# Kernel optimization log

Hardware: AMD Instinct MI355X
Metric: run time of the kernel (lower is better)

Reference implementation:

```python
import jax, jax.numpy as jnp
import numpy as np

B, S, D, H = 4, 1024, 1024, 16
DH = D // H  # head dim = 64


def setup_inputs() -> dict:
    key = jax.random.key(0)
    k0, k1, k2 = jax.random.split(key, 3)
    x = jax.random.normal(k0, (B, S, D), dtype=jnp.float32)
    c_attn_w = jax.random.normal(k1, (D, 3 * D), dtype=jnp.float32) * 0.02
    c_attn_b = jnp.zeros((3 * D,), dtype=jnp.float32)
    c_proj_w = jax.random.normal(k2, (D, D), dtype=jnp.float32) * 0.02
    c_proj_b = jnp.zeros((D,), dtype=jnp.float32)
    return {"x": x, "c_attn_w": c_attn_w, "c_attn_b": c_attn_b,
            "c_proj_w": c_proj_w, "c_proj_b": c_proj_b}


def reference(x, c_attn_w, c_attn_b, c_proj_w, c_proj_b):
    b, s, d = x.shape
    # Conv1D (GPT-2 style): out = x @ W + b, fused QKV
    qkv = jnp.einsum('bsd,de->bse', x, c_attn_w) + c_attn_b
    q, k, v = jnp.split(qkv, 3, axis=-1)
    # split heads -> [b, h, s, dh]
    q = q.reshape(b, s, H, DH).transpose(0, 2, 1, 3)
    k = k.reshape(b, s, H, DH).transpose(0, 2, 1, 3)
    v = v.reshape(b, s, H, DH).transpose(0, 2, 1, 3)
    # scaled scores with causal future mask (triu above diagonal -> -inf)
    w = jnp.einsum('bhqd,bhkd->bhqk', q, k) / jnp.sqrt(jnp.asarray(DH, x.dtype))
    future = jnp.triu(jnp.ones((s, s), dtype=bool), k=1)
    w = jnp.where(future[None, None, :, :], jnp.asarray(-jnp.inf, w.dtype), w)
    p = jax.nn.softmax(w, axis=-1)
    a = jnp.einsum('bhqk,bhkd->bhqd', p, v)
    # merge heads -> [b, s, d]
    a = a.transpose(0, 2, 1, 3).reshape(b, s, d)
    # output projection (Conv1D)
    out = jnp.einsum('bsd,de->bse', a, c_proj_w) + c_proj_b
    return out
```

## Files before the change

kernel.cpp:

```cpp
#include <hip/hip_runtime.h>
#include <math.h>

#define BB 4
#define SS 1024
#define DD 1024
#define HH 16
#define DHH 64

typedef short bf16x8 __attribute__((ext_vector_type(8)));
typedef float f32x4 __attribute__((ext_vector_type(4)));

__device__ __forceinline__ unsigned short f2bf(float f) {
    unsigned u = __float_as_uint(f);
    u += 0x7fffu + ((u >> 16) & 1u);
    return (unsigned short)(u >> 16);
}

__device__ __forceinline__ void glds16(const void* g, void* l) {
    __builtin_amdgcn_global_load_lds(
        (const __attribute__((address_space(1))) unsigned int*)g,
        (__attribute__((address_space(3))) unsigned int*)l, 16, 0, 0);
}

#define WAITCNT_VM(n)  (0xF70 | (n))
#define WAITCNT_LGKM0  (0xC07F)

__device__ __forceinline__ int swz(int row, int col) {
    return ((((col >> 4) ^ (row >> 2)) & 3) << 4) | (col & 15);
}

__global__ __launch_bounds__(256) void prologue_kernel(
    const float* __restrict__ x, const float* __restrict__ w1,
    const float* __restrict__ w2, unsigned short* __restrict__ Xb,
    unsigned short* __restrict__ W1t, unsigned short* __restrict__ W2t)
{
    __shared__ float tile[64][65];
    const int bx = blockIdx.x;
    if (bx < 4096) {
        int i = bx * 256 + threadIdx.x;
        float4 v = ((const float4*)x)[i];
        ushort4 o = { f2bf(v.x), f2bf(v.y), f2bf(v.z), f2bf(v.w) };
        ((ushort4*)Xb)[i] = o;
        return;
    }
    const float* W; unsigned short* Wt; int N, n0, k0;
    if (bx < 4864) {
        int id = bx - 4096; W = w1; Wt = W1t; N = 3072;
        n0 = (id % 48) * 64; k0 = (id / 48) * 64;
    } else {
        int id = bx - 4864; W = w2; Wt = W2t; N = 1024;
        n0 = (id & 15) * 64; k0 = (id >> 4) * 64;
    }
    int c = threadIdx.x & 63, r0 = threadIdx.x >> 6;
    #pragma unroll
    for (int i = 0; i < 16; ++i) {
        int r = r0 + i * 4;
        tile[r][c] = W[(size_t)(k0 + r) * N + n0 + c];
    }
    __syncthreads();
    #pragma unroll
    for (int i = 0; i < 16; ++i) {
        int r = r0 + i * 4;
        Wt[(size_t)(n0 + r) * 1024 + k0 + c] = f2bf(tile[c][r]);
    }
}

__global__ __launch_bounds__(256) void gemm_mfma(
    const unsigned short* __restrict__ A,
    const unsigned short* __restrict__ Bt,
    const float* __restrict__ bias,
    unsigned short* __restrict__ Cout,
    unsigned short* __restrict__ Vt,
    int N, int K)
{
    __shared__ unsigned short smem[24576];

    const int t = threadIdx.x;
    const int lane = t & 63;
    const int w = t >> 6;
    const int l15 = lane & 15, quad = lane >> 4;
    const int bm = blockIdx.y * 128, bn = blockIdx.x * 128;

    const int fragoff = l15 * K + quad * 8;

    const f32x4 zero4 = {0.f, 0.f, 0.f, 0.f};
    f32x4 acc[4][4];
    #pragma unroll
    for (int i = 0; i < 4; ++i)
        #pragma unroll
        for (int j = 0; j < 4; ++j) acc[i][j] = zero4;

    const unsigned short* Abase = A  + (size_t)bm * K + fragoff;
    const unsigned short* Bbase = Bt + (size_t)bn * K + fragoff;

    const int R = K / 32;

    auto issue = [&](int k, int b) {
        #pragma unroll
        for (int g2 = 0; g2 < 2; ++g2) {
            int g = w * 2 + g2;
            glds16(Abase + (size_t)(g * 16) * K + k * 32,
                   &smem[b * 8192 + g * 512]);
            glds16(Bbase + (size_t)(g * 16) * K + k * 32,
                   &smem[b * 8192 + 4096 + g * 512]);
        }
    };

    issue(0, 0);
    issue(1, 1);
    for (int k = 0; k < R; ++k) {
        if (k + 2 < R) {
            issue(k + 2, (k + 2) % 3);
            __builtin_amdgcn_s_waitcnt(WAITCNT_VM(8));
        } else if (k + 1 < R) {
            __builtin_amdgcn_s_waitcnt(WAITCNT_VM(4));
        } else {
            __builtin_amdgcn_s_waitcnt(WAITCNT_VM(0));
        }
        __builtin_amdgcn_s_barrier();

        bf16x8 af[4], bfr[4];
        #pragma unroll
        for (int mi = 0; mi < 4; ++mi)
            af[mi] = *(const bf16x8*)&smem[(k % 3) * 8192 + ((w >> 1) * 4 + mi) * 512 + lane * 8];
        #pragma unroll
        for (int nj = 0; nj < 4; ++nj)
            bfr[nj] = *(const bf16x8*)&smem[(k % 3) * 8192 + 4096 + ((w & 1) * 4 + nj) * 512 + lane * 8];
        #pragma unroll
        for (int mi = 0; mi < 4; ++mi)
            #pragma unroll
            for (int nj = 0; nj < 4; ++nj)
                acc[mi][nj] = __builtin_amdgcn_mfma_f32_16x16x32_bf16(
                    af[mi], bfr[nj], acc[mi][nj], 0, 0, 0);

        __builtin_amdgcn_s_barrier();
    }

    const int wm = (w >> 1) * 64;
    const int wn = (w & 1) * 64;
    float bv[4];
    #pragma unroll
    for (int nj = 0; nj < 4; ++nj) bv[nj] = bias[bn + wn + nj * 16 + l15];

    if (bn >= 2048) {
        #pragma unroll
        for (int mi = 0; mi < 4; ++mi)
            #pragma unroll
            for (int nj = 0; nj < 4; ++nj)
                #pragma unroll
                for (int r = 0; r < 4; ++r)
                    smem[(wn + nj * 16 + l15) * 136 + wm + mi * 16 + quad * 4 + r] =
                        f2bf(acc[mi][nj][r] + bv[nj]);
        __syncthreads();
        int b = bm >> 10, s0 = bm & 1023;
        int h0 = (bn - 2048) >> 6;
        #pragma unroll
        for (int i = 0; i < 8; ++i) {
            int flat = i * 2048 + t * 8;
            int ci = flat >> 7;
            int s8 = flat & 127;
            int h = h0 + (ci >> 6), dh = ci & 63;
            *(bf16x8*)&Vt[(((size_t)b * 16 + h) * 64 + dh) * 1024 + s0 + s8] =
                *(const bf16x8*)&smem[ci * 136 + s8];
        }
    } else {
        #pragma unroll
        for (int mi = 0; mi < 4; ++mi)
            #pragma unroll
            for (int nj = 0; nj < 4; ++nj)
                #pragma unroll
                for (int r = 0; r < 4; ++r)
                    smem[(wm + mi * 16 + quad * 4 + r) * 128 + wn + nj * 16 + l15] =
                        f2bf(acc[mi][nj][r] + bv[nj]);
        __syncthreads();
        #pragma unroll
        for (int i = 0; i < 8; ++i) {
            int off = i * 2048 + t * 8;
            int row = off >> 7, col = off & 127;
            *(bf16x8*)&Cout[(size_t)(bm + row) * N + bn + col] = *(const bf16x8*)&smem[off];
        }
    }
}

__global__ __launch_bounds__(256) void gemm2_mfma(
    const unsigned short* __restrict__ A,
    const unsigned short* __restrict__ Bt,
    const float* __restrict__ bias,
    float* __restrict__ C,
    int N, int K)
{
    __shared__ unsigned short smem[18432];

    const int t = threadIdx.x;
    const int lane = t & 63;
    const int w = t >> 6;
    const int l15 = lane & 15, quad = lane >> 4;
    const int bm = blockIdx.y * 64, bn = blockIdx.x * 128;

    const int fragoff = l15 * K + quad * 8;

    const f32x4 zero4 = {0.f, 0.f, 0.f, 0.f};
    f32x4 acc[2][4];
    #pragma unroll
    for (int i = 0; i < 2; ++i)
        #pragma unroll
        for (int j = 0; j < 4; ++j) acc[i][j] = zero4;

    const unsigned short* Abase = A  + (size_t)bm * K + fragoff;
    const unsigned short* Bbase = Bt + (size_t)bn * K + fragoff;

    const int R = K / 32;

    auto issue = [&](int k, int b) {
        glds16(Abase + (size_t)(w * 16) * K + k * 32,
               &smem[b * 6144 + w * 512]);
        #pragma unroll
        for (int g2 = 0; g2 < 2; ++g2) {
            int g = w * 2 + g2;
            glds16(Bbase + (size_t)(g * 16) * K + k * 32,
                   &smem[b * 6144 + 2048 + g * 512]);
        }
    };

    issue(0, 0);
    issue(1, 1);
    for (int k = 0; k < R; ++k) {
        if (k + 2 < R) {
            issue(k + 2, (k + 2) % 3);
            __builtin_amdgcn_s_waitcnt(WAITCNT_VM(6));
        } else if (k + 1 < R) {
            __builtin_amdgcn_s_waitcnt(WAITCNT_VM(3));
        } else {
            __builtin_amdgcn_s_waitcnt(WAITCNT_VM(0));
        }
        __builtin_amdgcn_s_barrier();

        bf16x8 af[2], bfr[4];
        #pragma unroll
        for (int mi = 0; mi < 2; ++mi)
            af[mi] = *(const bf16x8*)&smem[(k % 3) * 6144 + ((w >> 1) * 2 + mi) * 512 + lane * 8];
        #pragma unroll
        for (int nj = 0; nj < 4; ++nj)
            bfr[nj] = *(const bf16x8*)&smem[(k % 3) * 6144 + 2048 + ((w & 1) * 4 + nj) * 512 + lane * 8];
        #pragma unroll
        for (int mi = 0; mi < 2; ++mi)
            #pragma unroll
            for (int nj = 0; nj < 4; ++nj)
                acc[mi][nj] = __builtin_amdgcn_mfma_f32_16x16x32_bf16(
                    af[mi], bfr[nj], acc[mi][nj], 0, 0, 0);

        __builtin_amdgcn_s_barrier();
    }

    const int wm = (w >> 1) * 32;
    const int wn = (w & 1) * 64;
    float bv[4];
    #pragma unroll
    for (int nj = 0; nj < 4; ++nj) bv[nj] = bias[bn + wn + nj * 16 + l15];

    float* fs = (float*)smem;
    #pragma unroll
    for (int mi = 0; mi < 2; ++mi)
        #pragma unroll
        for (int nj = 0; nj < 4; ++nj)
            #pragma unroll
            for (int r = 0; r < 4; ++r)
                fs[(wm + mi * 16 + quad * 4 + r) * 128 + wn + nj * 16 + l15] =
                    acc[mi][nj][r] + bv[nj];
    __syncthreads();
    #pragma unroll
    for (int i = 0; i < 8; ++i) {
        int off = i * 256 + t;
        int row = off >> 5, col = (off & 31) * 4;
        *(float4*)&C[(size_t)(bm + row) * N + bn + col] =
            *(const float4*)&fs[row * 128 + col];
    }
}

__device__ __forceinline__ void attn_tile_step8(
    bf16x8 q0, bf16x8 q1, float* lsum, f32x4* o,
    const unsigned short (*Ks)[80], const unsigned short (*VsT)[80],
    unsigned short (*Ps)[80],
    int wq, int l15, int quad, bool diag)
{
    const f32x4 zero4 = {0.f, 0.f, 0.f, 0.f};
    f32x4 s[4];
    #pragma unroll
    for (int nj = 0; nj < 4; ++nj) {
        int n = nj * 16 + l15;
        f32x4 sa = zero4;
        bf16x8 b0 = *(const bf16x8*)&Ks[n][swz(n, quad * 8)];
        bf16x8 b1 = *(const bf16x8*)&Ks[n][swz(n, 32 + quad * 8)];
        sa = __builtin_amdgcn_mfma_f32_16x16x32_bf16(q0, b0, sa, 0, 0, 0);
        sa = __builtin_amdgcn_mfma_f32_16x16x32_bf16(q1, b1, sa, 0, 0, 0);
        s[nj] = sa;
    }
    const float scale = 0.125f;

    #pragma unroll
    for (int nj = 0; nj < 4; ++nj)
        #pragma unroll
        for (int r = 0; r < 4; ++r) {
            float sv = s[nj][r] * scale;
            if (diag && (nj * 16 + l15) > (wq * 16 + quad * 4 + r)) sv = -INFINITY;
            float p = __expf(sv);
            lsum[r] += p;
            int qloc = wq * 16 + quad * 4 + r;
            Ps[qloc][swz(qloc, nj * 16 + l15)] = f2bf(p);
        }

    #pragma unroll
    for (int kk = 0; kk < 2; ++kk) {
        int m = wq * 16 + l15;
        bf16x8 pa = *(const bf16x8*)&Ps[m][swz(m, kk * 32 + quad * 8)];
        #pragma unroll
        for (int nj = 0; nj < 4; ++nj) {
            int n = nj * 16 + l15;
            bf16x8 vb = *(const bf16x8*)&VsT[n][swz(n, kk * 32 + quad * 8)];
            o[nj] = __builtin_amdgcn_mfma_f32_16x16x32_bf16(pa, vb, o[nj], 0, 0, 0);
        }
    }
}

__global__ __launch_bounds__(512) void attn_mfma(
    const unsigned short* __restrict__ qkv,
    const unsigned short* __restrict__ Vt,
    unsigned short* __restrict__ aout)
{
    __shared__ unsigned short Ks[64][80];
    __shared__ unsigned short VsT[64][80];
    __shared__ unsigned short Ps[2][64][80];

    const int t = threadIdx.x;
    const int lane = t & 63;
    const int wave = t >> 6;
    const int wq = wave & 3;
    const int tile = wave >> 2;
    const int l15 = lane & 15, quad = lane >> 4;
    const int qlo = blockIdx.x;
    const int qhi = 15 - qlo;
    const int qb = tile ? qhi : qlo;
    const int bh = blockIdx.y;
    const int b = bh >> 4, h = bh & 15;
    const size_t qkvbase = (size_t)b * SS * 3072;
    const f32x4 zero4 = {0.f, 0.f, 0.f, 0.f};

    bf16x8 qf0, qf1;
    {
        const unsigned short* p = qkv + qkvbase +
            (size_t)(qb * 64 + wq * 16 + l15) * 3072 + h * 64 + quad * 8;
        qf0 = *(const bf16x8*)p;
        qf1 = *(const bf16x8*)(p + 32);
    }

    float lsum[4];
    f32x4 o[4];
    #pragma unroll
    for (int r = 0; r < 4; ++r) lsum[r] = 0.f;
    #pragma unroll
    for (int nj = 0; nj < 4; ++nj) o[nj] = zero4;

    const int sr = t >> 3, scc = (t & 7) * 8;
    const unsigned short* kgp = qkv + qkvbase + 1024 + h * 64 + (size_t)sr * 3072 + scc;
    const unsigned short* vgp = Vt + ((size_t)bh * 64 + sr) * 1024 + scc;
    bf16x8 kreg, vreg;

    kreg = *(const bf16x8*)(kgp);
    vreg = *(const bf16x8*)(vgp);

    for (int kb = 0; kb <= qhi; ++kb) {
        __builtin_amdgcn_s_barrier();
        *(bf16x8*)&Ks[sr][swz(sr, scc)] = kreg;
        *(bf16x8*)&VsT[sr][swz(sr, scc)] = vreg;
        if (kb < qhi) {
            kreg = *(const bf16x8*)(kgp + (size_t)(kb + 1) * 64 * 3072);
            vreg = *(const bf16x8*)(vgp + (kb + 1) * 64);
        }
        __builtin_amdgcn_s_waitcnt(WAITCNT_LGKM0);
        __builtin_amdgcn_s_barrier();

        if (kb <= qb)
            attn_tile_step8(qf0, qf1, lsum, o, Ks, VsT, Ps[tile],
                            wq, l15, quad, kb == qb);
    }

    #pragma unroll
    for (int off = 1; off < 16; off <<= 1)
        #pragma unroll
        for (int r = 0; r < 4; ++r)
            lsum[r] += __shfl_xor(lsum[r], off);

    #pragma unroll
    for (int r = 0; r < 4; ++r) {
        float inv = 1.0f / lsum[r];
        int rloc = wq * 16 + quad * 4 + r;
        size_t ob = ((size_t)b * SS + qb * 64 + rloc) * 1024 + h * 64;
        #pragma unroll
        for (int nj = 0; nj < 4; ++nj)
            aout[ob + nj * 16 + l15] = f2bf(o[nj][r] * inv);
    }
}

extern "C" void kernel_launch(void* const* d_in, const int* in_sizes, int n_in,
                              void* d_out, int out_size, void* d_ws, size_t ws_size,
                              hipStream_t stream)
{
    const float* x     = (const float*)d_in[0];
    const float* wqkv  = (const float*)d_in[1];
    const float* bqkv  = (const float*)d_in[2];
    const float* wproj = (const float*)d_in[3];
    const float* bproj = (const float*)d_in[4];
    float* out = (float*)d_out;

    unsigned short* ws   = (unsigned short*)d_ws;
    unsigned short* Xb   = ws;
    unsigned short* W1t  = Xb  + (size_t)4096 * 1024;
    unsigned short* W2t  = W1t + (size_t)3072 * 1024;
    unsigned short* qkv  = W2t + (size_t)1024 * 1024;
    unsigned short* Vt   = qkv + (size_t)4096 * 3072;
    unsigned short* abuf = Vt  + (size_t)64 * 64 * 1024;

    prologue_kernel<<<5120, 256, 0, stream>>>(x, wqkv, wproj, Xb, W1t, W2t);

    gemm_mfma<<<dim3(3072 / 128, 4096 / 128), 256, 0, stream>>>(
        Xb, W1t, bqkv, qkv, Vt, 3072, 1024);

    attn_mfma<<<dim3(8, 64), 512, 0, stream>>>(qkv, Vt, abuf);

    gemm2_mfma<<<dim3(1024 / 128, 4096 / 64), 256, 0, stream>>>(
        abuf, W2t, bproj, out, 1024, 1024);
}
```

Before: 182.5 us.

## Rewrite QKV GEMM with 256x256 tiles, 8 waves, swizzled LDS and phased prefetch

The QKV projection GEMM moves from 128x128 tiles with 4 waves to 256x256 tiles with 8 waves. Each wave now computes 128x64 of output, which raises operand reuse per LDS load. LDS is XOR-swizzled to avoid bank conflicts. Loads for the next K tile are spread across four compute phases with s_setprio around the MFMA bursts, so fetches overlap compute. The costs are a much larger LDS footprint and only 192 workgroups on a chip with 256 CUs, so part of the GPU may sit idle (tail/occupancy risk).

```diff
diff --git a/kernel.cpp b/kernel.cpp
--- a/kernel.cpp
+++ b/kernel.cpp
@@ -65,7 +65,7 @@
     }
 }
 
-__global__ __launch_bounds__(256) void gemm_mfma(
+__global__ __launch_bounds__(512, 2) void gemm_mfma(
     const unsigned short* __restrict__ A,
     const unsigned short* __restrict__ Bt,
     const float* __restrict__ bias,
@@ -73,111 +73,141 @@
     unsigned short* __restrict__ Vt,
     int N, int K)
 {
-    __shared__ unsigned short smem[24576];
+    __shared__ unsigned short smem[65536];
 
     const int t = threadIdx.x;
     const int lane = t & 63;
     const int w = t >> 6;
     const int l15 = lane & 15, quad = lane >> 4;
-    const int bm = blockIdx.y * 128, bn = blockIdx.x * 128;
-
-    const int fragoff = l15 * K + quad * 8;
+    const int wr = w >> 2, wc = w & 3;
+    const int bm = blockIdx.y * 256, bn = blockIdx.x * 256;
+
+    const int sl_ca = ((lane & 7) ^ (lane >> 3)) << 4;
+    const unsigned short* sl_base =
+        (sl_ca < 64) ? (A + (size_t)bm * K) : (Bt + (size_t)bn * K);
+    const int sl_k = (sl_ca & 63) >> 1;
+
+    auto stage = [&](int tile, int kh, int rh) {
+        #pragma unroll
+        for (int j = 0; j < 2; ++j) {
+            int row = rh * 128 + j * 64 + w * 8 + (lane >> 3);
+            glds16(sl_base + (size_t)row * K + tile * 64 + kh * 32 + sl_k,
+                   &smem[((tile & 1) * 2 + kh) * 16384 +
+                         rh * 8192 + j * 4096 + w * 512]);
+        }
+    };
 
     const f32x4 zero4 = {0.f, 0.f, 0.f, 0.f};
-    f32x4 acc[4][4];
-    #pragma unroll
-    for (int i = 0; i < 4; ++i)
+    f32x4 acc[8][4];
+    #pragma unroll
+    for (int i = 0; i < 8; ++i)
         #pragma unroll
         for (int j = 0; j < 4; ++j) acc[i][j] = zero4;
 
-    const unsigned short* Abase = A  + (size_t)bm * K + fragoff;
-    const unsigned short* Bbase = Bt + (size_t)bn * K + fragoff;
-
-    const int R = K / 32;
-
-    auto issue = [&](int k, int b) {
-        #pragma unroll
-        for (int g2 = 0; g2 < 2; ++g2) {
-            int g = w * 2 + g2;
-            glds16(Abase + (size_t)(g * 16) * K + k * 32,
-                   &smem[b * 8192 + g * 512]);
-            glds16(Bbase + (size_t)(g * 16) * K + k * 32,
-                   &smem[b * 8192 + 4096 + g * 512]);
-        }
-    };
-
-    issue(0, 0);
-    issue(1, 1);
-    for (int k = 0; k < R; ++k) {
-        if (k + 2 < R) {
-            issue(k + 2, (k + 2) % 3);
-            __builtin_amdgcn_s_waitcnt(WAITCNT_VM(8));
-        } else if (k + 1 < R) {
-            __builtin_amdgcn_s_waitcnt(WAITCNT_VM(4));
-        } else {
-            __builtin_amdgcn_s_waitcnt(WAITCNT_VM(0));
-        }
-        __builtin_amdgcn_s_barrier();
-
-        bf16x8 af[4], bfr[4];
-        #pragma unroll
-        for (int mi = 0; mi < 4; ++mi)
-            af[mi] = *(const bf16x8*)&smem[(k % 3) * 8192 + ((w >> 1) * 4 + mi) * 512 + lane * 8];
-        #pragma unroll
-        for (int nj = 0; nj < 4; ++nj)
-            bfr[nj] = *(const bf16x8*)&smem[(k % 3) * 8192 + 4096 + ((w & 1) * 4 + nj) * 512 + lane * 8];
-        #pragma unroll
-        for (int mi = 0; mi < 4; ++mi)
-            #pragma unroll
-            for (int nj = 0; nj < 4; ++nj)
-                acc[mi][nj] = __builtin_amdgcn_mfma_f32_16x16x32_bf16(
-                    af[mi], bfr[nj], acc[mi][nj], 0, 0, 0);
-
-        __builtin_amdgcn_s_barrier();
-    }
-
-    const int wm = (w >> 1) * 64;
-    const int wn = (w & 1) * 64;
+    const int T = K / 64;
+
+    stage(0, 0, 0); stage(0, 0, 1); stage(0, 1, 0); stage(0, 1, 1);
+    stage(1, 0, 0); stage(1, 0, 1);
+    __builtin_amdgcn_s_waitcnt(WAITCNT_VM(4));
+
+    bf16x8 bfr[4];
+    for (int tt = 0; tt < T; ++tt) {
+        const int buf = tt & 1;
+        #pragma unroll
+        for (int ph = 0; ph < 4; ++ph) {
+            const int kh = ph >> 1;
+            const int mh = ph & 1;
+            __builtin_amdgcn_s_barrier();
+            __builtin_amdgcn_sched_barrier(0);
+
+            bf16x8 af[4];
+            #pragma unroll
+            for (int i = 0; i < 4; ++i) {
+                int row = wr * 128 + (mh * 4 + i) * 16 + l15;
+                int byte = (row << 7) + (quad << 4);
+                byte ^= (l15 & 7) << 4;
+                af[i] = *(const bf16x8*)&smem[(buf * 2 + kh) * 16384 + (byte >> 1)];
+            }
+            if (mh == 0) {
+                #pragma unroll
+                for (int nj = 0; nj < 4; ++nj) {
+                    int row = wc * 64 + nj * 16 + l15;
+                    int byte = (row << 7) + 64 + (quad << 4);
+                    byte ^= (l15 & 7) << 4;
+                    bfr[nj] = *(const bf16x8*)&smem[(buf * 2 + kh) * 16384 + (byte >> 1)];
+                }
+            }
+
+            if (ph == 0)      { if (tt + 1 < T) stage(tt + 1, 1, 0); }
+            else if (ph == 1) { if (tt + 1 < T) stage(tt + 1, 1, 1); }
+            else if (ph == 2) { if (tt + 2 < T) stage(tt + 2, 0, 0); }
+            else              { if (tt + 2 < T) stage(tt + 2, 0, 1); }
+
+            __builtin_amdgcn_s_setprio(1);
+            #pragma unroll
+            for (int i = 0; i < 4; ++i)
+                #pragma unroll
+                for (int nj = 0; nj < 4; ++nj)
+                    acc[mh * 4 + i][nj] = __builtin_amdgcn_mfma_f32_16x16x32_bf16(
+                        af[i], bfr[nj], acc[mh * 4 + i][nj], 0, 0, 0);
+            __builtin_amdgcn_s_setprio(0);
+        }
+        if (tt + 2 < T)      __builtin_amdgcn_s_waitcnt(WAITCNT_VM(4));
+        else if (tt + 1 < T) __builtin_amdgcn_s_waitcnt(WAITCNT_VM(0));
+    }
+
+    __syncthreads();
+
     float bv[4];
     #pragma unroll
-    for (int nj = 0; nj < 4; ++nj) bv[nj] = bias[bn + wn + nj * 16 + l15];
+    for (int nj = 0; nj < 4; ++nj) bv[nj] = bias[bn + wc * 64 + nj * 16 + l15];
 
     if (bn >= 2048) {
         #pragma unroll
-        for (int mi = 0; mi < 4; ++mi)
+        for (int mi = 0; mi < 8; ++mi)
             #pragma unroll
             for (int nj = 0; nj < 4; ++nj)
                 #pragma unroll
-                for (int r = 0; r < 4; ++r)
-                    smem[(wn + nj * 16 + l15) * 136 + wm + mi * 16 + quad * 4 + r] =
+                for (int r = 0; r < 4; ++r) {
+                    int row = wr * 128 + mi * 16 + quad * 4 + r;
+                    int col = wc * 64 + nj * 16 + l15;
+                    smem[col * 256 + (row ^ (((col >> 2) & 3) << 4))] =
                         f2bf(acc[mi][nj][r] + bv[nj]);
+                }
         __syncthreads();
         int b = bm >> 10, s0 = bm & 1023;
         int h0 = (bn - 2048) >> 6;
         #pragma unroll
-        for (int i = 0; i < 8; ++i) {
-            int flat = i * 2048 + t * 8;
-            int ci = flat >> 7;
-            int s8 = flat & 127;
-            int h = h0 + (ci >> 6), dh = ci & 63;
-            *(bf16x8*)&Vt[(((size_t)b * 16 + h) * 64 + dh) * 1024 + s0 + s8] =
-                *(const bf16x8*)&smem[ci * 136 + s8];
+        for (int it = 0; it < 16; ++it) {
+            int chunk = it * 512 + t;
+            int col = chunk >> 5;
+            int r8 = (chunk & 31) * 8;
+            bf16x8 val = *(const bf16x8*)&smem[col * 256 +
+                         (r8 ^ (((col >> 2) & 3) << 4))];
+            int h = h0 + (col >> 6), dh = col & 63;
+            *(bf16x8*)&Vt[(((size_t)b * 16 + h) * 64 + dh) * 1024 + s0 + r8] = val;
         }
     } else {
         #pragma unroll
-        for (int mi = 0; mi < 4; ++mi)
+        for (int mi = 0; mi < 8; ++mi)
             #pragma unroll
             for (int nj = 0; nj < 4; ++nj)
                 #pragma unroll
-                for (int r = 0; r < 4; ++r)
-                    smem[(wm + mi * 16 + quad * 4 + r) * 128 + wn + nj * 16 + l15] =
+                for (int r = 0; r < 4; ++r) {
+                    int row = wr * 128 + mi * 16 + quad * 4 + r;
+                    int col = wc * 64 + nj * 16 + l15;
+                    smem[row * 256 + (col ^ (((row >> 2) & 3) << 4))] =
                         f2bf(acc[mi][nj][r] + bv[nj]);
+                }
         __syncthreads();
         #pragma unroll
-        for (int i = 0; i < 8; ++i) {
-            int off = i * 2048 + t * 8;
-            int row = off >> 7, col = off & 127;
-            *(bf16x8*)&Cout[(size_t)(bm + row) * N + bn + col] = *(const bf16x8*)&smem[off];
+        for (int it = 0; it < 16; ++it) {
+            int chunk = it * 512 + t;
+            int row = chunk >> 5;
+            int col = (chunk & 31) * 8;
+            bf16x8 val = *(const bf16x8*)&smem[row * 256 +
+                         (col ^ (((row >> 2) & 3) << 4))];
+            *(bf16x8*)&Cout[(size_t)(bm + row) * N + bn + col] = val;
         }
     }
 }
@@ -422,7 +452,7 @@
 
     prologue_kernel<<<5120, 256, 0, stream>>>(x, wqkv, wproj, Xb, W1t, W2t);
 
-    gemm_mfma<<<dim3(3072 / 128, 4096 / 128), 256, 0, stream>>>(
+    gemm_mfma<<<dim3(3072 / 256, 4096 / 256), 512, 0, stream>>>(
         Xb, W1t, bqkv, qkv, Vt, 3072, 1024);
 
     attn_mfma<<<dim3(8, 64), 512, 0, stream>>>(qkv, Vt, abuf);
```

Result: faster. 167.8 us (-8.1%).
